# Optimization experiments

Hardware: AMD Instinct MI355X
Metric: run time of the kernel (lower is better)

The kernel has to match this reference:

```python
import jax, jax.numpy as jnp
import numpy as np

N_LAYERS = 2
N_COEF = 5
IN_DIM = 256
LN_EPS = 1e-6  # flax LayerNorm default


def jacobi_design(x, a, n):
    """Jacobi polynomials P_0..P_{n-1}^{(a,a)}(x). x: [...], returns [..., n]."""
    Ps = [jnp.ones_like(x)]
    if n > 1:
        Ps.append((a + 1.0) * x)
    for k in range(2, n):
        t = 2.0 * k + 2.0 * a
        A = 2.0 * k * (k + 2.0 * a) * (t - 2.0)
        B = (t - 1.0) * t * (t - 2.0)
        C = 2.0 * (k + a - 1.0) ** 2 * t
        Ps.append((B * x * Ps[-1] - C * Ps[-2]) / A)
    return jnp.stack(Ps, axis=-1)


def setup_inputs() -> dict:
    key = jax.random.key(0)
    k1, k2 = jax.random.split(key)
    x = jax.random.normal(k1, (8192, IN_DIM), dtype=jnp.float32)
    coefs = jax.random.normal(k2, (N_LAYERS, IN_DIM, IN_DIM, N_COEF), dtype=jnp.float32) * 0.03
    alphas = jnp.zeros((N_LAYERS,), dtype=jnp.float32)      # alpha_arctanh init zeros
    ln_scale = jnp.ones((N_LAYERS, IN_DIM), dtype=jnp.float32)
    ln_bias = jnp.zeros((N_LAYERS, IN_DIM), dtype=jnp.float32)
    return {"x": x, "coefs": coefs, "alphas": alphas, "ln_scale": ln_scale, "ln_bias": ln_bias}


def reference(x, coefs, alphas, ln_scale, ln_bias):
    h = x  # [B, D]
    for l in range(N_LAYERS):
        # LayerNorm
        mu = jnp.mean(h, axis=-1, keepdims=True)
        var = jnp.mean(jnp.square(h - mu), axis=-1, keepdims=True)
        hn = (h - mu) * jax.lax.rsqrt(var + LN_EPS) * ln_scale[l] + ln_bias[l]
        # KANLayer: Jacobi design matrix on tanh-mapped input
        a = jnp.tanh(alphas[l])
        dm = jacobi_design(jnp.tanh(hn), a, N_COEF)  # [B, D, C]
        # resid_scale=0, spline_scale=1, dropout inactive -> y = mean_i einsum
        in_dim = hn.shape[-1]
        h = jnp.einsum('bic,ioc->bo', dm, coefs[l]) / in_dim  # [B, D]
    return h
```

## Files before the change

kernel.cpp:

```cpp
#include <hip/hip_runtime.h>

#define D 256
#define NB 8192
#define NKC 128
#define PANEL (NKC * 512)

#define SXX_STRIDE 264
#define SXX_ELEMS (32 * SXX_STRIDE)
#define SMEM_BYTES (SXX_ELEMS * 2 + 65536)

typedef __bf16 bf16;
typedef bf16 bf16x8 __attribute__((ext_vector_type(8)));
typedef bf16 bf16x4 __attribute__((ext_vector_type(4)));
typedef float f32x4 __attribute__((ext_vector_type(4)));

__device__ __forceinline__ void glds16(const bf16* g, bf16* l) {
    __builtin_amdgcn_global_load_lds((const __attribute__((address_space(1))) void*)g,
                                     (__attribute__((address_space(3))) void*)l, 16, 0, 0);
}

__device__ __forceinline__ float fast_tanh(float x) {
    float e = __expf(2.f * x);
    return 1.f - 2.f / (e + 1.f);
}

__global__ __launch_bounds__(256) void pack_kernel(const float* __restrict__ coefs,
                                                   bf16* __restrict__ Wt,
                                                   float* __restrict__ beta) {
    __shared__ float t[64 * 65];
    __shared__ float accs[4][64];
    int b = blockIdx.x;
    if (b < 128) {
        int l = b >> 6, rem = b & 63;
        int c = (rem >> 4) + 1, tl = rem & 15;
        int plane = (c == 1) ? 0 : (c == 4) ? 1 : (c == 2) ? 2 : 3;
        int i0 = (tl >> 2) * 64, o0 = (tl & 3) * 64;

        for (int j = threadIdx.x; j < 4096; j += 256) {
            int i = j >> 6, o = j & 63;
            t[i * 65 + o] = coefs[(((size_t)(l * 256 + i0 + i)) * 256 + (o0 + o)) * 5 + c];
        }
        __syncthreads();
        bf16* dst = Wt + (size_t)l * (4 * PANEL)
                       + ((size_t)(tl & 3) * NKC + (plane * 256 + i0) / 8) * 512;
        for (int j = threadIdx.x; j < 4096; j += 256) {
            int il = j & 7, o = (j >> 3) & 63, ih = j >> 9;
            dst[j] = (bf16)t[(ih * 8 + il) * 65 + o];
        }
    } else {
        int lidx = b - 128;
        int l = lidx >> 2, o0 = (lidx & 3) * 64;
        int o = threadIdx.x & 63, ig = threadIdx.x >> 6;
        float sum = 0.f;
        for (int m = 0; m < 64; ++m) {
            int i = ig * 64 + m;
            sum += coefs[(((size_t)(l * 256 + i)) * 256 + (o0 + o)) * 5 + 0];
        }
        accs[ig][o] = sum;
        __syncthreads();
        if (threadIdx.x < 64)
            beta[l * 256 + o0 + threadIdx.x] = accs[0][threadIdx.x] + accs[1][threadIdx.x]
                                             + accs[2][threadIdx.x] + accs[3][threadIdx.x];
    }
}

template <int PH>
__device__ __forceinline__ void gemm_half(f32x4 (&acc)[2][4], const bf16* __restrict__ Wp,
                                          const bf16* sxx, bf16* sW, int l, float a1,
                                          float rB0, float rB1, float rB2,
                                          float rC0, float rC1, float rC2) {
    bf16x8 afn[2];
#pragma unroll
    for (int it = 0; it < 16; ++it) {
        if (it == 15) __builtin_amdgcn_s_waitcnt(0x0F70);
        else          __builtin_amdgcn_s_waitcnt(0x0F74);
        const bf16* sWb = sW + (it & 1) * 2048;

        bf16x8 bfr[4];
#pragma unroll
        for (int tn = 0; tn < 4; ++tn)
            bfr[tn] = *(const bf16x8*)(sWb + (l >> 4) * 512 + (16 * tn + (l & 15)) * 8);

        bf16x8 af[2];
        if ((it & 1) == 0) {
            const int j  = it >> 1;
            const int i0 = j * 32 + (l >> 4) * 8;
#pragma unroll
            for (int tm = 0; tm < 2; ++tm) {
                bf16x8 xv = *(const bf16x8*)(sxx + (16 * tm + (l & 15)) * SXX_STRIDE + i0);
#pragma unroll
                for (int jj = 0; jj < 8; ++jj) {
                    float x  = (float)xv[jj];
                    float P1 = a1 * x;
                    float P2 = rB0 * x * P1 - rC0;
                    float P3 = rB1 * x * P2 - rC1 * P1;
                    float PA, PB;
                    if (PH == 0) { PA = P1; PB = rB2 * x * P3 - rC2 * P2; }
                    else         { PA = P2; PB = P3; }
                    af[tm][jj]  = (bf16)PA;
                    afn[tm][jj] = (bf16)PB;
                }
            }
        } else {
            af[0] = afn[0];
            af[1] = afn[1];
        }

#pragma unroll
        for (int tm = 0; tm < 2; ++tm)
#pragma unroll
            for (int tn = 0; tn < 4; ++tn)
                acc[tm][tn] = __builtin_amdgcn_mfma_f32_16x16x32_bf16(
                    af[tm], bfr[tn], acc[tm][tn], 0, 0, 0);

        if (it < 14) {
            __builtin_amdgcn_s_waitcnt(0xC07F);
            __builtin_amdgcn_sched_barrier(0);
            const int itp   = it + 2;
            const int chunk = (PH * 2 + (itp & 1)) * 8 + (itp >> 1);
            bf16* dst = sW + (it & 1) * 2048;
#pragma unroll
            for (int t = 0; t < 4; ++t)
                glds16(Wp + chunk * 2048 + t * 512 + l * 8, dst + t * 512);
        }
    }
}

__global__ __launch_bounds__(512, 2) void fused2_kernel(
    const float* __restrict__ x, const float* __restrict__ ln_scale,
    const float* __restrict__ ln_bias, const float* __restrict__ alphas,
    const bf16* __restrict__ Wt, const float* __restrict__ beta,
    float* __restrict__ out) {
    extern __shared__ __align__(16) bf16 smem[];
    bf16* sxx  = smem;
    bf16* stag = smem + SXX_ELEMS;

    const int tid = threadIdx.x;
    const int l   = tid & 63;
    const int w   = tid >> 6;
    const int g   = w >> 1, p = w & 1;
    const int slab = blockIdx.x;

    bf16* sW = stag + w * 4096;

#pragma unroll
    for (int L = 0; L < 2; ++L) {
        const float* scale = ln_scale + L * D;
        const float* biasp = ln_bias + L * D;
        const bf16*  Wl    = Wt + (size_t)L * 4 * PANEL;
        const float* bet   = beta + L * D;

        const float a  = tanhf(alphas[L]);
        const float a1 = a + 1.f;
        float rB[3], rC[3];
#pragma unroll
        for (int k = 2; k < 5; k++) {
            float tk  = 2.f * k + 2.f * a;
            float iAk = 1.f / (2.f * k * (k + 2.f * a) * (tk - 2.f));
            rB[k - 2] = (tk - 1.f) * tk * (tk - 2.f) * iAk;
            rC[k - 2] = 2.f * (k + a - 1.f) * (k + a - 1.f) * tk * iAk;
        }

        float4 sc4 = ((const float4*)scale)[l];
        float4 bi4 = ((const float4*)biasp)[l];
        float scv[4] = {sc4.x, sc4.y, sc4.z, sc4.w};
        float biv[4] = {bi4.x, bi4.y, bi4.z, bi4.w};

#pragma unroll
        for (int rr = 0; rr < 4; ++rr) {
            int lr = w * 4 + rr;
            float4 v;
            if (L == 0) {
                v = ((const float4*)(x + ((size_t)slab * 32 + lr) * D))[l];
            } else {
                const float* hp = (const float*)(stag + (size_t)(l >> 4) * 8192);
                v = *(const float4*)(hp + lr * 64 + (l & 15) * 4);
            }
            float s  = v.x + v.y + v.z + v.w;
            float ss = v.x * v.x + v.y * v.y + v.z * v.z + v.w * v.w;
#pragma unroll
            for (int off = 32; off > 0; off >>= 1) {
                s  += __shfl_down(s, off);
                ss += __shfl_down(ss, off);
            }
            s  = __shfl(s, 0);
            ss = __shfl(ss, 0);
            float mu   = s * (1.f / D);
            float rstd = rsqrtf(ss * (1.f / D) - mu * mu + 1e-6f);
            float hv[4] = {v.x, v.y, v.z, v.w};
            bf16x4 o;
#pragma unroll
            for (int e = 0; e < 4; ++e)
                o[e] = (bf16)fast_tanh((hv[e] - mu) * rstd * scv[e] + biv[e]);
            *(bf16x4*)(sxx + lr * SXX_STRIDE + 4 * l) = o;
        }
        __syncthreads();

        const bf16* Wp = Wl + (size_t)g * PANEL;
#pragma unroll
        for (int itp = 0; itp < 2; ++itp) {
            bf16* dst = sW + itp * 2048;
            const int chunk = (p * 2 + itp) * 8;
#pragma unroll
            for (int t = 0; t < 4; ++t)
                glds16(Wp + chunk * 2048 + t * 512 + l * 8, dst + t * 512);
        }

        f32x4 acc[2][4] = {};
        if (p == 0) gemm_half<0>(acc, Wp, sxx, sW, l, a1, rB[0], rB[1], rB[2], rC[0], rC[1], rC[2]);
        else        gemm_half<1>(acc, Wp, sxx, sW, l, a1, rB[0], rB[1], rB[2], rC[0], rC[1], rC[2]);

        if (p == 1) {
            f32x4* dumpr = (f32x4*)(stag + (size_t)w * 4096);
#pragma unroll
            for (int tm = 0; tm < 2; ++tm)
#pragma unroll
                for (int tn = 0; tn < 4; ++tn)
                    dumpr[(tm * 4 + tn) * 64 + l] = acc[tm][tn];
        }
        __syncthreads();

        if (p == 0) {
            f32x4* part = (f32x4*)(stag + (size_t)(w + 1) * 4096);
            if (L == 0) {
                float* hp = (float*)(stag + (size_t)w * 4096);
#pragma unroll
                for (int tm = 0; tm < 2; ++tm)
#pragma unroll
                    for (int tn = 0; tn < 4; ++tn) {
                        int lc = 16 * tn + (l & 15);
                        float bv = bet[g * 64 + lc] * (1.f / 256.f);
                        f32x4 v = acc[tm][tn] + part[(tm * 4 + tn) * 64 + l];
                        int lr0 = 16 * tm + (l >> 4) * 4;
#pragma unroll
                        for (int r = 0; r < 4; ++r)
                            hp[(lr0 + r) * 64 + lc] = v[r] * (1.f / 256.f) + bv;
                    }
            } else {
#pragma unroll
                for (int tm = 0; tm < 2; ++tm)
#pragma unroll
                    for (int tn = 0; tn < 4; ++tn) {
                        int gc = g * 64 + 16 * tn + (l & 15);
                        float bv = bet[gc] * (1.f / 256.f);
                        f32x4 v = acc[tm][tn] + part[(tm * 4 + tn) * 64 + l];
                        int gr = slab * 32 + 16 * tm + (l >> 4) * 4;
#pragma unroll
                        for (int r = 0; r < 4; ++r)
                            out[(size_t)(gr + r) * D + gc] = v[r] * (1.f / 256.f) + bv;
                    }
            }
        }
        __syncthreads();
    }
}

extern "C" void kernel_launch(void* const* d_in, const int* in_sizes, int n_in,
                              void* d_out, int out_size, void* d_ws, size_t ws_size,
                              hipStream_t stream) {
    const float* x        = (const float*)d_in[0];
    const float* coefs    = (const float*)d_in[1];
    const float* alphas   = (const float*)d_in[2];
    const float* ln_scale = (const float*)d_in[3];
    const float* ln_bias  = (const float*)d_in[4];
    float* out = (float*)d_out;

    char* ws = (char*)d_ws;
    bf16*  Wt   = (bf16*)ws;
    float* beta = (float*)(ws + 1048576);

    hipFuncSetAttribute((const void*)fused2_kernel,
                        hipFuncAttributeMaxDynamicSharedMemorySize, SMEM_BYTES);

    pack_kernel<<<136, 256, 0, stream>>>(coefs, Wt, beta);
    fused2_kernel<<<256, 512, SMEM_BYTES, stream>>>(x, ln_scale, ln_bias, alphas,
                                                    Wt, beta, out);
}
```

Before: 95.82 us.

## Precompute Jacobi design matrix into LDS once instead of per-wave recomputation

Each row's Jacobi polynomials P1..P4 are now computed once during the LayerNorm pass and stored as a bf16 A-operand panel in shared memory, in chunk-major order. The GEMM loop then reads A fragments directly from LDS instead of recomputing the recurrence from tanh inputs inside every wave. This removes redundant VALU work that was repeated across the column-group waves, at the cost of a larger LDS footprint (128×260 bf16 instead of 32×264). The weight chunk indexing is changed to match the new K ordering.

New measurement: 100.8 us. +5.2%, slower.

```diff
diff --git a/kernel.cpp b/kernel.cpp
--- a/kernel.cpp
+++ b/kernel.cpp
@@ -5,9 +5,9 @@
 #define NKC 128
 #define PANEL (NKC * 512)
 
-#define SXX_STRIDE 264
-#define SXX_ELEMS (32 * SXX_STRIDE)
-#define SMEM_BYTES (SXX_ELEMS * 2 + 65536)
+#define ACH 260
+#define A_ELEMS (128 * ACH)
+#define SMEM_BYTES ((A_ELEMS + 8 * 4096) * 2)
 
 typedef __bf16 bf16;
 typedef bf16 bf16x8 __attribute__((ext_vector_type(8)));
@@ -64,76 +64,14 @@
     }
 }
 
-template <int PH>
-__device__ __forceinline__ void gemm_half(f32x4 (&acc)[2][4], const bf16* __restrict__ Wp,
-                                          const bf16* sxx, bf16* sW, int l, float a1,
-                                          float rB0, float rB1, float rB2,
-                                          float rC0, float rC1, float rC2) {
-    bf16x8 afn[2];
-#pragma unroll
-    for (int it = 0; it < 16; ++it) {
-        if (it == 15) __builtin_amdgcn_s_waitcnt(0x0F70);
-        else          __builtin_amdgcn_s_waitcnt(0x0F74);
-        const bf16* sWb = sW + (it & 1) * 2048;
-
-        bf16x8 bfr[4];
-#pragma unroll
-        for (int tn = 0; tn < 4; ++tn)
-            bfr[tn] = *(const bf16x8*)(sWb + (l >> 4) * 512 + (16 * tn + (l & 15)) * 8);
-
-        bf16x8 af[2];
-        if ((it & 1) == 0) {
-            const int j  = it >> 1;
-            const int i0 = j * 32 + (l >> 4) * 8;
-#pragma unroll
-            for (int tm = 0; tm < 2; ++tm) {
-                bf16x8 xv = *(const bf16x8*)(sxx + (16 * tm + (l & 15)) * SXX_STRIDE + i0);
-#pragma unroll
-                for (int jj = 0; jj < 8; ++jj) {
-                    float x  = (float)xv[jj];
-                    float P1 = a1 * x;
-                    float P2 = rB0 * x * P1 - rC0;
-                    float P3 = rB1 * x * P2 - rC1 * P1;
-                    float PA, PB;
-                    if (PH == 0) { PA = P1; PB = rB2 * x * P3 - rC2 * P2; }
-                    else         { PA = P2; PB = P3; }
-                    af[tm][jj]  = (bf16)PA;
-                    afn[tm][jj] = (bf16)PB;
-                }
-            }
-        } else {
-            af[0] = afn[0];
-            af[1] = afn[1];
-        }
-
-#pragma unroll
-        for (int tm = 0; tm < 2; ++tm)
-#pragma unroll
-            for (int tn = 0; tn < 4; ++tn)
-                acc[tm][tn] = __builtin_amdgcn_mfma_f32_16x16x32_bf16(
-                    af[tm], bfr[tn], acc[tm][tn], 0, 0, 0);
-
-        if (it < 14) {
-            __builtin_amdgcn_s_waitcnt(0xC07F);
-            __builtin_amdgcn_sched_barrier(0);
-            const int itp   = it + 2;
-            const int chunk = (PH * 2 + (itp & 1)) * 8 + (itp >> 1);
-            bf16* dst = sW + (it & 1) * 2048;
-#pragma unroll
-            for (int t = 0; t < 4; ++t)
-                glds16(Wp + chunk * 2048 + t * 512 + l * 8, dst + t * 512);
-        }
-    }
-}
-
 __global__ __launch_bounds__(512, 2) void fused2_kernel(
     const float* __restrict__ x, const float* __restrict__ ln_scale,
     const float* __restrict__ ln_bias, const float* __restrict__ alphas,
     const bf16* __restrict__ Wt, const float* __restrict__ beta,
     float* __restrict__ out) {
     extern __shared__ __align__(16) bf16 smem[];
-    bf16* sxx  = smem;
-    bf16* stag = smem + SXX_ELEMS;
+    bf16* aL   = smem;
+    bf16* stag = smem + A_ELEMS;
 
     const int tid = threadIdx.x;
     const int l   = tid & 63;
@@ -188,11 +126,23 @@
             float mu   = s * (1.f / D);
             float rstd = rsqrtf(ss * (1.f / D) - mu * mu + 1e-6f);
             float hv[4] = {v.x, v.y, v.z, v.w};
-            bf16x4 o;
-#pragma unroll
-            for (int e = 0; e < 4; ++e)
-                o[e] = (bf16)fast_tanh((hv[e] - mu) * rstd * scv[e] + biv[e]);
-            *(bf16x4*)(sxx + lr * SXX_STRIDE + 4 * l) = o;
+
+            bf16x4 o1, o2, o3, o4;
+#pragma unroll
+            for (int e = 0; e < 4; ++e) {
+                float xx = fast_tanh((hv[e] - mu) * rstd * scv[e] + biv[e]);
+                float P1 = a1 * xx;
+                float P2 = rB[0] * xx * P1 - rC[0];
+                float P3 = rB[1] * xx * P2 - rC[1] * P1;
+                float P4 = rB[2] * xx * P3 - rC[2] * P2;
+                o1[e] = (bf16)P1; o2[e] = (bf16)P2;
+                o3[e] = (bf16)P3; o4[e] = (bf16)P4;
+            }
+            size_t base = (size_t)(l >> 1) * ACH + lr * 8 + 4 * (l & 1);
+            *(bf16x4*)(aL + base + (size_t)(0 * 32) * ACH) = o1;
+            *(bf16x4*)(aL + base + (size_t)(1 * 32) * ACH) = o4;
+            *(bf16x4*)(aL + base + (size_t)(2 * 32) * ACH) = o2;
+            *(bf16x4*)(aL + base + (size_t)(3 * 32) * ACH) = o3;
         }
         __syncthreads();
 
@@ -200,15 +150,49 @@
 #pragma unroll
         for (int itp = 0; itp < 2; ++itp) {
             bf16* dst = sW + itp * 2048;
-            const int chunk = (p * 2 + itp) * 8;
+            const int chunk = p * 16 + itp;
 #pragma unroll
             for (int t = 0; t < 4; ++t)
                 glds16(Wp + chunk * 2048 + t * 512 + l * 8, dst + t * 512);
         }
 
         f32x4 acc[2][4] = {};
-        if (p == 0) gemm_half<0>(acc, Wp, sxx, sW, l, a1, rB[0], rB[1], rB[2], rC[0], rC[1], rC[2]);
-        else        gemm_half<1>(acc, Wp, sxx, sW, l, a1, rB[0], rB[1], rB[2], rC[0], rC[1], rC[2]);
+#pragma unroll
+        for (int it = 0; it < 16; ++it) {
+            if (it == 15) __builtin_amdgcn_s_waitcnt(0x0F70);
+            else          __builtin_amdgcn_s_waitcnt(0x0F74);
+            const bf16* sWb = sW + (it & 1) * 2048;
+
+            bf16x8 bfr[4];
+#pragma unroll
+            for (int tn = 0; tn < 4; ++tn)
+                bfr[tn] = *(const bf16x8*)(sWb + (l >> 4) * 512 + (16 * tn + (l & 15)) * 8);
+
+            bf16x8 af[2];
+            {
+                const int cc = (p * 16 + it) * 4 + (l >> 4);
+#pragma unroll
+                for (int tm = 0; tm < 2; ++tm)
+                    af[tm] = *(const bf16x8*)(aL + (size_t)cc * ACH + (16 * tm + (l & 15)) * 8);
+            }
+
+#pragma unroll
+            for (int tm = 0; tm < 2; ++tm)
+#pragma unroll
+                for (int tn = 0; tn < 4; ++tn)
+                    acc[tm][tn] = __builtin_amdgcn_mfma_f32_16x16x32_bf16(
+                        af[tm], bfr[tn], acc[tm][tn], 0, 0, 0);
+
+            if (it < 14) {
+                __builtin_amdgcn_s_waitcnt(0xC07F);
+                __builtin_amdgcn_sched_barrier(0);
+                const int chunk = p * 16 + it + 2;
+                bf16* dst = sW + (it & 1) * 2048;
+#pragma unroll
+                for (int t = 0; t < 4; ++t)
+                    glds16(Wp + chunk * 2048 + t * 512 + l * 8, dst + t * 512);
+            }
+        }
 
         if (p == 1) {
             f32x4* dumpr = (f32x4*)(stag + (size_t)w * 4096);
```
